# Kernel optimization log

Measured on AMD Instinct MI355X. Metric: run time of the kernel, lower is better.

Reference implementation:

```python
import jax, jax.numpy as jnp
import numpy as np

B, S, H = 16, 512, 768
NH, DH = 12, 64  # heads, head dim (H = NH*DH)
E = 8            # number of experts


def setup_inputs() -> dict:
    key = jax.random.key(0)
    ks = jax.random.split(key, 9)
    w_scale = 1.0 / np.sqrt(H).astype(np.float32)
    return {
        "hidden_states": jax.random.normal(ks[0], (B, S, H), jnp.float32),
        "attention_mask": jnp.zeros((B, 1, 1, S), jnp.float32),
        "Wq": jax.random.normal(ks[1], (E, H, H), jnp.float32) * w_scale,
        "bq": jnp.zeros((E, H), jnp.float32),
        "Wk": jax.random.normal(ks[2], (E, H, H), jnp.float32) * w_scale,
        "bk": jnp.zeros((E, H), jnp.float32),
        "Wv": jax.random.normal(ks[3], (E, H, H), jnp.float32) * w_scale,
        "bv": jnp.zeros((E, H), jnp.float32),
        "expert_idx": jax.random.randint(ks[4], (B,), 0, E, jnp.int64),
    }


def reference(hidden_states, attention_mask, Wq, bq, Wk, bk, Wv, bv, expert_idx):
    b, s, h = hidden_states.shape

    def proj(W, bias):
        # Per-sample expert selection: math-equivalent to computing all experts
        # then slice_for_expert, but gathers weights instead of activations.
        Wg = W[expert_idx]            # [B, H_out, H_in]
        bg = bias[expert_idx]         # [B, H_out]
        y = jnp.einsum('bsd,bod->bso', hidden_states, Wg) + bg[:, None, :]
        return y.reshape(b, s, NH, DH).transpose(0, 2, 1, 3)  # [B, NH, S, DH]

    q = proj(Wq, bq)
    k = proj(Wk, bk)
    v = proj(Wv, bv)

    scores = jnp.einsum('bhqd,bhkd->bhqk', q, k) / np.sqrt(DH).astype(np.float32)
    scores = scores + attention_mask
    probs = jax.nn.softmax(scores, axis=-1)  # dropout p=0.0 (eval)
    ctx = jnp.einsum('bhqk,bhkd->bhqd', probs, v)
    return ctx.transpose(0, 2, 1, 3).reshape(b, s, h)
```

## Files before the change

kernel.cpp:

```cpp
#include <hip/hip_runtime.h>
#include <hip/hip_bf16.h>
#include <stdint.h>

typedef __bf16 bf16;
typedef bf16 bf16x8 __attribute__((ext_vector_type(8)));
typedef bf16 bf16x4 __attribute__((ext_vector_type(4)));
typedef float f32x4 __attribute__((ext_vector_type(4)));

#define MFMA_16x16x32(a, b, c) __builtin_amdgcn_mfma_f32_16x16x32_bf16((a), (b), (c), 0, 0, 0)

constexpr int B = 16, S = 512, H = 768, NH = 12, DH = 64;
constexpr long NHID = (long)B * S * H;
constexpr long NW = (long)8 * H * H;

constexpr size_t XB_OFF = 0;
constexpr size_t XB_SZ  = (size_t)NHID * 2;
constexpr size_t W_SZ   = (size_t)NW * 2;
constexpr size_t WQ_OFF = XB_OFF + XB_SZ;
constexpr size_t WK_OFF = WQ_OFF + W_SZ;
constexpr size_t WV_OFF = WK_OFF + W_SZ;
constexpr size_t PROJ_SZ = (size_t)B * NH * S * DH * 2;
constexpr size_t QB_OFF = WV_OFF + W_SZ;
constexpr size_t KB_OFF = QB_OFF + PROJ_SZ;
constexpr size_t VB_OFF = KB_OFF + PROJ_SZ;
constexpr size_t WS_NEED = VB_OFF + PROJ_SZ;

__global__ void cvt_all(const float* __restrict__ x,
                        const float* __restrict__ wq, const float* __restrict__ wk,
                        const float* __restrict__ wv,
                        bf16* __restrict__ xb, bf16* __restrict__ wqb,
                        bf16* __restrict__ wkb, bf16* __restrict__ wvb) {
  long i = ((long)blockIdx.x * blockDim.x + threadIdx.x) * 8;
  const float* src;
  bf16* dst;
  long off;
  if (i < NHID)               { src = x;  dst = xb;  off = i; }
  else if (i < NHID + NW)     { src = wq; dst = wqb; off = i - NHID; }
  else if (i < NHID + 2 * NW) { src = wk; dst = wkb; off = i - NHID - NW; }
  else if (i < NHID + 3 * NW) { src = wv; dst = wvb; off = i - NHID - 2 * NW; }
  else return;
  const float4* sp = reinterpret_cast<const float4*>(src + off);
  float4 a = sp[0], b = sp[1];
  bf16x8 o;
  o[0] = (bf16)a.x; o[1] = (bf16)a.y; o[2] = (bf16)a.z; o[3] = (bf16)a.w;
  o[4] = (bf16)b.x; o[5] = (bf16)b.y; o[6] = (bf16)b.z; o[7] = (bf16)b.w;
  *reinterpret_cast<bf16x8*>(dst + off) = o;
}

__global__ __launch_bounds__(512, 2) void proj_gemm(
    const bf16* __restrict__ Xb,
    const bf16* __restrict__ Wqb, const bf16* __restrict__ Wkb, const bf16* __restrict__ Wvb,
    const float* __restrict__ bq, const float* __restrict__ bk, const float* __restrict__ bv,
    const int* __restrict__ eidx,
    bf16* __restrict__ Qb, bf16* __restrict__ Kb, bf16* __restrict__ Vb)
{
  __shared__ __align__(16) bf16 As[2][256 * 32];
  __shared__ __align__(16) bf16 Bs[2][128 * 32];

  const int xcd = blockIdx.x & 7;
  const int bi  = blockIdx.x >> 3;
  const int b   = xcd * 2 + (bi / 36);
  const int rem = bi % 36;
  const int m0  = (rem / 18) * 256;
  const int gy  = rem % 18;
  const int proj = gy / 6;
  const int n0 = (gy % 6) * 128;
  const int e = eidx[b];

  const bf16* W = (proj == 0 ? Wqb : (proj == 1 ? Wkb : Wvb)) + (size_t)e * H * H;
  const float* bias = (proj == 0 ? bq : (proj == 1 ? bk : bv)) + (size_t)e * H;
  bf16* Out = (proj == 0 ? Qb : (proj == 1 ? Kb : Vb));

  const int tid = threadIdx.x;
  const int lane = tid & 63;
  const int wave = tid >> 6;
  const int wm = wave >> 1, wn = wave & 1;
  const int r = lane & 15, lg = lane >> 4;

  const bf16* Abase = Xb + ((size_t)b * S + m0) * H;
  const bf16* Bbase = W + (size_t)n0 * H;

  const int srow = lane >> 2;
  const int sg = ((lane & 3) ^ ((lane >> 3) & 3)) * 8;

  auto stage = [&](int kt, int pb) {
    const int k0 = kt * 32;
#pragma unroll
    for (int i = 0; i < 2; ++i) {
      const int seg = wave * 2 + i;
      const bf16* ga = Abase + (size_t)(seg * 16 + srow) * H + k0 + sg;
      __builtin_amdgcn_global_load_lds(
          (const __attribute__((address_space(1))) void*)ga,
          (__attribute__((address_space(3))) void*)(&As[pb][seg * 512]), 16, 0, 0);
    }
    const bf16* gb = Bbase + (size_t)(wave * 16 + srow) * H + k0 + sg;
    __builtin_amdgcn_global_load_lds(
        (const __attribute__((address_space(1))) void*)gb,
        (__attribute__((address_space(3))) void*)(&Bs[pb][wave * 512]), 16, 0, 0);
  };

  f32x4 acc[4][4] = {};

  stage(0, 0);
  __syncthreads();

  const int sz = (r >> 1) & 3;

  int buf = 0;
#pragma unroll 1
  for (int kt = 0; kt < 24; ++kt) {
    if (kt < 23) stage(kt + 1, buf ^ 1);

    bf16x8 af[4], bfr[4];
#pragma unroll
    for (int mi = 0; mi < 4; ++mi)
      af[mi] = *reinterpret_cast<const bf16x8*>(
          &As[buf][(wm * 64 + mi * 16 + r) * 32 + ((lg ^ sz) * 8)]);
#pragma unroll
    for (int ni = 0; ni < 4; ++ni)
      bfr[ni] = *reinterpret_cast<const bf16x8*>(
          &Bs[buf][(wn * 64 + ni * 16 + r) * 32 + ((lg ^ sz) * 8)]);
#pragma unroll
    for (int mi = 0; mi < 4; ++mi)
#pragma unroll
      for (int ni = 0; ni < 4; ++ni)
        acc[mi][ni] = MFMA_16x16x32(af[mi], bfr[ni], acc[mi][ni]);

    __syncthreads();
    buf ^= 1;
  }

  if (proj != 2) {
#pragma unroll
    for (int ni = 0; ni < 4; ++ni) {
      const int col = n0 + wn * 64 + ni * 16 + r;
      const int nh = col >> 6, dh = col & 63;
      const float bb = bias[col];
      bf16* orow = Out + ((size_t)b * NH + nh) * S * DH + dh;
#pragma unroll
      for (int mi = 0; mi < 4; ++mi) {
#pragma unroll
        for (int rr = 0; rr < 4; ++rr) {
          const int srow2 = m0 + wm * 64 + mi * 16 + lg * 4 + rr;
          orow[(size_t)srow2 * DH] = (bf16)(acc[mi][ni][rr] + bb);
        }
      }
    }
  } else {
#pragma unroll
    for (int ni = 0; ni < 4; ++ni) {
      const int col = n0 + wn * 64 + ni * 16 + r;
      const int nh = col >> 6, dh = col & 63;
      const float bb = bias[col];
      bf16* orow = Out + ((size_t)b * NH + nh) * DH * S + (size_t)dh * S;
#pragma unroll
      for (int mi = 0; mi < 4; ++mi) {
        bf16x4 v;
#pragma unroll
        for (int rr = 0; rr < 4; ++rr) v[rr] = (bf16)(acc[mi][ni][rr] + bb);
        *reinterpret_cast<bf16x4*>(orow + m0 + wm * 64 + mi * 16 + lg * 4) = v;
      }
    }
  }
}

__global__ __launch_bounds__(256, 4) void attn_kernel(
    const bf16* __restrict__ Qb, const bf16* __restrict__ Kb, const bf16* __restrict__ VTb,
    const float* __restrict__ mask, float* __restrict__ out)
{
  __shared__ __align__(16) bf16 Ks[2][64 * 64];
  __shared__ __align__(16) bf16 Vs[2][64 * 64];
  __shared__ float maskS[512];

  const int x = blockIdx.x;
  const int xcd = x & 7;
  const int grp = x >> 3;
  const int qblk = grp & 7;
  const int bh = (grp >> 3) * 8 + xcd;
  const int b = bh / NH;
  const int h = bh % NH;
  const int tid = threadIdx.x;
  const int wave = tid >> 6;
  const int lane = tid & 63;
  const int r = lane & 15, lg = lane >> 4;
  const int q0 = qblk * 64 + wave * 16;

  const bf16* Q  = Qb  + (size_t)bh * S * DH;
  const bf16* K  = Kb  + (size_t)bh * S * DH;
  const bf16* VT = VTb + (size_t)bh * DH * S;

  for (int i = tid; i < S; i += 256) maskS[i] = mask[b * S + i];

  const int srowoff = lane >> 3;
  const int sg = (lane & 7) ^ srowoff;

  auto stage = [&](int kt, int buf) {
    const int kb = kt * 64;
#pragma unroll
    for (int i = 0; i < 2; ++i) {
      const int c = wave * 2 + i;
      const int row = c * 8 + srowoff;
      const bf16* gk = K + (size_t)(kb + row) * DH + sg * 8;
      __builtin_amdgcn_global_load_lds(
          (const __attribute__((address_space(1))) void*)gk,
          (__attribute__((address_space(3))) void*)(&Ks[buf][c * 512]), 16, 0, 0);
      const bf16* gv = VT + (size_t)row * S + kb + sg * 8;
      __builtin_amdgcn_global_load_lds(
          (const __attribute__((address_space(1))) void*)gv,
          (__attribute__((address_space(3))) void*)(&Vs[buf][c * 512]), 16, 0, 0);
    }
  };

  const bf16x8 qf0 = *reinterpret_cast<const bf16x8*>(&Q[(size_t)(q0 + r) * DH + lg * 8]);
  const bf16x8 qf1 = *reinterpret_cast<const bf16x8*>(&Q[(size_t)(q0 + r) * DH + 32 + lg * 8]);

  stage(0, 0);
  __syncthreads();

  float m = -3.0e38f, l = 0.0f;
  f32x4 ctx[4] = {};
  int buf = 0;

#pragma unroll 1
  for (int kt = 0; kt < 8; ++kt) {
    const int kb = kt * 64;
    if (kt < 7) stage(kt + 1, buf ^ 1);

    f32x4 sa[4];
#pragma unroll
    for (int t = 0; t < 4; ++t) {
      const int row = t * 16 + r;
      const int sw = row & 7;
      bf16x8 kf0 = *reinterpret_cast<const bf16x8*>(&Ks[buf][row * 64 + ((lg ^ sw) * 8)]);
      bf16x8 kf1 = *reinterpret_cast<const bf16x8*>(&Ks[buf][row * 64 + (((lg + 4) ^ sw) * 8)]);
      f32x4 a = {};
      a = MFMA_16x16x32(kf0, qf0, a);
      a = MFMA_16x16x32(kf1, qf1, a);
      sa[t] = a;
    }

    float tmax = -3.0e38f;
#pragma unroll
    for (int t = 0; t < 4; ++t)
#pragma unroll
      for (int rr = 0; rr < 4; ++rr) {
        float s = sa[t][rr] * 0.125f + maskS[kb + t * 16 + lg * 4 + rr];
        sa[t][rr] = s;
        tmax = fmaxf(tmax, s);
      }
    tmax = fmaxf(tmax, __shfl_xor(tmax, 16));
    tmax = fmaxf(tmax, __shfl_xor(tmax, 32));
    const float mnew = fmaxf(m, tmax);
    const float scale = __expf(m - mnew);
    m = mnew;
    float ps = 0.f;
#pragma unroll
    for (int t = 0; t < 4; ++t)
#pragma unroll
      for (int rr = 0; rr < 4; ++rr) {
        float p = __expf(sa[t][rr] - mnew);
        sa[t][rr] = p;
        ps += p;
      }
    l = l * scale + ps;
#pragma unroll
    for (int dt = 0; dt < 4; ++dt) ctx[dt] *= scale;

#pragma unroll
    for (int kc = 0; kc < 2; ++kc) {
      bf16x8 pf;
      f32x4 p0 = sa[2 * kc], p1 = sa[2 * kc + 1];
      pf[0] = (bf16)p0[0]; pf[1] = (bf16)p0[1]; pf[2] = (bf16)p0[2]; pf[3] = (bf16)p0[3];
      pf[4] = (bf16)p1[0]; pf[5] = (bf16)p1[1]; pf[6] = (bf16)p1[2]; pf[7] = (bf16)p1[3];
      const int chunk_lo = kc * 4 + (lg >> 1);
      const int rem = (lg & 1) * 4;
#pragma unroll
      for (int dt = 0; dt < 4; ++dt) {
        const int row = dt * 16 + r;
        const int sw = row & 7;
        const bf16* vlo = &Vs[buf][row * 64 + ((chunk_lo ^ sw) * 8) + rem];
        const bf16* vhi = &Vs[buf][row * 64 + (((chunk_lo + 2) ^ sw) * 8) + rem];
        bf16x4 lo = *reinterpret_cast<const bf16x4*>(vlo);
        bf16x4 hi = *reinterpret_cast<const bf16x4*>(vhi);
        bf16x8 vf;
        vf[0] = lo[0]; vf[1] = lo[1]; vf[2] = lo[2]; vf[3] = lo[3];
        vf[4] = hi[0]; vf[5] = hi[1]; vf[6] = hi[2]; vf[7] = hi[3];
        ctx[dt] = MFMA_16x16x32(vf, pf, ctx[dt]);
      }
    }

    __syncthreads();
    buf ^= 1;
  }

  l += __shfl_xor(l, 16);
  l += __shfl_xor(l, 32);
  const float inv = 1.0f / l;

  float* obase = out + ((size_t)b * S + q0 + r) * H + h * DH;
#pragma unroll
  for (int dt = 0; dt < 4; ++dt) {
    float4 o;
    o.x = ctx[dt][0] * inv; o.y = ctx[dt][1] * inv;
    o.z = ctx[dt][2] * inv; o.w = ctx[dt][3] * inv;
    *reinterpret_cast<float4*>(obase + dt * 16 + lg * 4) = o;
  }
}

extern "C" void kernel_launch(void* const* d_in, const int* in_sizes, int n_in,
                              void* d_out, int out_size, void* d_ws, size_t ws_size,
                              hipStream_t stream) {
  const float* hidden = (const float*)d_in[0];
  const float* mask   = (const float*)d_in[1];
  const float* Wq = (const float*)d_in[2];
  const float* bq = (const float*)d_in[3];
  const float* Wk = (const float*)d_in[4];
  const float* bk = (const float*)d_in[5];
  const float* Wv = (const float*)d_in[6];
  const float* bv = (const float*)d_in[7];
  const int* eidx = (const int*)d_in[8];

  if (ws_size < WS_NEED) return;

  char* ws = (char*)d_ws;
  bf16* Xb  = (bf16*)(ws + XB_OFF);
  bf16* Wqb = (bf16*)(ws + WQ_OFF);
  bf16* Wkb = (bf16*)(ws + WK_OFF);
  bf16* Wvb = (bf16*)(ws + WV_OFF);
  bf16* Qbf = (bf16*)(ws + QB_OFF);
  bf16* Kbf = (bf16*)(ws + KB_OFF);
  bf16* Vbf = (bf16*)(ws + VB_OFF);
  float* out = (float*)d_out;

  cvt_all<<<9984, 256, 0, stream>>>(hidden, Wq, Wk, Wv, Xb, Wqb, Wkb, Wvb);
  proj_gemm<<<576, 512, 0, stream>>>(Xb, Wqb, Wkb, Wvb, bq, bk, bv, eidx,
                                     Qbf, Kbf, Vbf);
  attn_kernel<<<1536, 256, 0, stream>>>(Qbf, Kbf, Vbf, mask, out);
}
```

Measured before the change: 102.9 us.

## Retile projection GEMM to 128x192 with triple-buffered 64-wide K pipeline

Changes the projection GEMM tile from 256x128 to 128x192, which raises the grid from 576 to 768 blocks, and doubles the K step to 64 over 12 iterations. LDS staging moves from double to triple buffering, with two stages in flight and hand-written s_waitcnt vmcnt/s_barrier in place of __syncthreads. MFMA bursts are wrapped in s_setprio. The aim is to hide global-to-LDS latency better and balance the work across CUs. In exchange it uses more LDS per block, and the exact vmcnt counts are fragile.

```diff
diff --git a/kernel.cpp b/kernel.cpp
--- a/kernel.cpp
+++ b/kernel.cpp
@@ -54,17 +54,18 @@
     const int* __restrict__ eidx,
     bf16* __restrict__ Qb, bf16* __restrict__ Kb, bf16* __restrict__ Vb)
 {
-  __shared__ __align__(16) bf16 As[2][256 * 32];
-  __shared__ __align__(16) bf16 Bs[2][128 * 32];
+  __shared__ __align__(16) bf16 As[3][2 * 128 * 32];
+  __shared__ __align__(16) bf16 Bs[3][2 * 192 * 32];
 
   const int xcd = blockIdx.x & 7;
   const int bi  = blockIdx.x >> 3;
-  const int b   = xcd * 2 + (bi / 36);
-  const int rem = bi % 36;
-  const int m0  = (rem / 18) * 256;
-  const int gy  = rem % 18;
-  const int proj = gy / 6;
-  const int n0 = (gy % 6) * 128;
+  const int b   = xcd * 2 + (bi / 48);
+  const int rem = bi % 48;
+  const int mt  = rem / 12;
+  const int nt  = rem % 12;
+  const int m0  = mt * 128;
+  const int proj = nt >> 2;
+  const int n0  = (nt & 3) * 192;
   const int e = eidx[b];
 
   const bf16* W = (proj == 0 ? Wqb : (proj == 1 ? Wkb : Wvb)) + (size_t)e * H * H;
@@ -74,7 +75,7 @@
   const int tid = threadIdx.x;
   const int lane = tid & 63;
   const int wave = tid >> 6;
-  const int wm = wave >> 1, wn = wave & 1;
+  const int wm = wave >> 2, wn = wave & 3;
   const int r = lane & 15, lg = lane >> 4;
 
   const bf16* Abase = Xb + ((size_t)b * S + m0) * H;
@@ -84,56 +85,77 @@
   const int sg = ((lane & 3) ^ ((lane >> 3) & 3)) * 8;
 
   auto stage = [&](int kt, int pb) {
-    const int k0 = kt * 32;
+    const int k0 = kt * 64;
 #pragma unroll
     for (int i = 0; i < 2; ++i) {
-      const int seg = wave * 2 + i;
-      const bf16* ga = Abase + (size_t)(seg * 16 + srow) * H + k0 + sg;
+      const int u = wave * 2 + i;
+      const int kh = u >> 3, p = u & 7;
+      const bf16* ga = Abase + (size_t)(p * 16 + srow) * H + k0 + kh * 32 + sg;
       __builtin_amdgcn_global_load_lds(
           (const __attribute__((address_space(1))) void*)ga,
-          (__attribute__((address_space(3))) void*)(&As[pb][seg * 512]), 16, 0, 0);
-    }
-    const bf16* gb = Bbase + (size_t)(wave * 16 + srow) * H + k0 + sg;
-    __builtin_amdgcn_global_load_lds(
-        (const __attribute__((address_space(1))) void*)gb,
-        (__attribute__((address_space(3))) void*)(&Bs[pb][wave * 512]), 16, 0, 0);
+          (__attribute__((address_space(3))) void*)(&As[pb][u * 512]), 16, 0, 0);
+    }
+#pragma unroll
+    for (int i = 0; i < 3; ++i) {
+      const int u = wave * 3 + i;
+      const int kh = u / 12, p = u % 12;
+      const bf16* gb = Bbase + (size_t)(p * 16 + srow) * H + k0 + kh * 32 + sg;
+      __builtin_amdgcn_global_load_lds(
+          (const __attribute__((address_space(1))) void*)gb,
+          (__attribute__((address_space(3))) void*)(&Bs[pb][u * 512]), 16, 0, 0);
+    }
   };
 
-  f32x4 acc[4][4] = {};
+  f32x4 acc[4][3] = {};
 
   stage(0, 0);
-  __syncthreads();
+  stage(1, 1);
+  asm volatile("s_waitcnt vmcnt(5) lgkmcnt(0)\n\ts_barrier" ::: "memory");
 
   const int sz = (r >> 1) & 3;
 
-  int buf = 0;
+  int buf = 0, nb = 2;
 #pragma unroll 1
-  for (int kt = 0; kt < 24; ++kt) {
-    if (kt < 23) stage(kt + 1, buf ^ 1);
-
-    bf16x8 af[4], bfr[4];
-#pragma unroll
-    for (int mi = 0; mi < 4; ++mi)
-      af[mi] = *reinterpret_cast<const bf16x8*>(
-          &As[buf][(wm * 64 + mi * 16 + r) * 32 + ((lg ^ sz) * 8)]);
-#pragma unroll
-    for (int ni = 0; ni < 4; ++ni)
-      bfr[ni] = *reinterpret_cast<const bf16x8*>(
-          &Bs[buf][(wn * 64 + ni * 16 + r) * 32 + ((lg ^ sz) * 8)]);
-#pragma unroll
-    for (int mi = 0; mi < 4; ++mi)
-#pragma unroll
-      for (int ni = 0; ni < 4; ++ni)
-        acc[mi][ni] = MFMA_16x16x32(af[mi], bfr[ni], acc[mi][ni]);
-
-    __syncthreads();
-    buf ^= 1;
+  for (int t = 0; t < 12; ++t) {
+    if (t + 2 < 12) stage(t + 2, nb);
+
+    const bf16* Ab = &As[buf][0];
+    const bf16* Bb = &Bs[buf][0];
+#pragma unroll
+    for (int kh = 0; kh < 2; ++kh) {
+      bf16x8 bfr[3];
+#pragma unroll
+      for (int ni = 0; ni < 3; ++ni)
+        bfr[ni] = *reinterpret_cast<const bf16x8*>(
+            &Bb[kh * 6144 + (wn * 48 + ni * 16 + r) * 32 + ((lg ^ sz) * 8)]);
+#pragma unroll
+      for (int half = 0; half < 2; ++half) {
+        bf16x8 af0 = *reinterpret_cast<const bf16x8*>(
+            &Ab[kh * 4096 + (wm * 64 + (half * 2) * 16 + r) * 32 + ((lg ^ sz) * 8)]);
+        bf16x8 af1 = *reinterpret_cast<const bf16x8*>(
+            &Ab[kh * 4096 + (wm * 64 + (half * 2 + 1) * 16 + r) * 32 + ((lg ^ sz) * 8)]);
+        __builtin_amdgcn_s_setprio(1);
+#pragma unroll
+        for (int ni = 0; ni < 3; ++ni) {
+          acc[half * 2][ni]     = MFMA_16x16x32(af0, bfr[ni], acc[half * 2][ni]);
+          acc[half * 2 + 1][ni] = MFMA_16x16x32(af1, bfr[ni], acc[half * 2 + 1][ni]);
+        }
+        __builtin_amdgcn_s_setprio(0);
+      }
+    }
+
+    if (t < 10)
+      asm volatile("s_waitcnt vmcnt(5) lgkmcnt(0)\n\ts_barrier" ::: "memory");
+    else if (t == 10)
+      asm volatile("s_waitcnt vmcnt(0) lgkmcnt(0)\n\ts_barrier" ::: "memory");
+    buf = (buf == 2) ? 0 : buf + 1;
+    nb  = (nb == 2) ? 0 : nb + 1;
   }
 
   if (proj != 2) {
 #pragma unroll
-    for (int ni = 0; ni < 4; ++ni) {
-      const int col = n0 + wn * 64 + ni * 16 + r;
+    for (int ni = 0; ni < 3; ++ni) {
+      const int col = n0 + wn * 48 + ni * 16 + r;
       const int nh = col >> 6, dh = col & 63;
       const float bb = bias[col];
       bf16* orow = Out + ((size_t)b * NH + nh) * S * DH + dh;
@@ -148,8 +170,8 @@
     }
   } else {
 #pragma unroll
-    for (int ni = 0; ni < 4; ++ni) {
-      const int col = n0 + wn * 64 + ni * 16 + r;
+    for (int ni = 0; ni < 3; ++ni) {
+      const int col = n0 + wn * 48 + ni * 16 + r;
       const int nh = col >> 6, dh = col & 63;
       const float bb = bias[col];
       bf16* orow = Out + ((size_t)b * NH + nh) * DH * S + (size_t)dh * S;
@@ -333,7 +355,7 @@
   float* out = (float*)d_out;
 
   cvt_all<<<9984, 256, 0, stream>>>(hidden, Wq, Wk, Wv, Xb, Wqb, Wkb, Wvb);
-  proj_gemm<<<576, 512, 0, stream>>>(Xb, Wqb, Wkb, Wvb, bq, bk, bv, eidx,
+  proj_gemm<<<768, 512, 0, stream>>>(Xb, Wqb, Wkb, Wvb, bq, bk, bv, eidx,
                                      Qbf, Kbf, Vbf);
   attn_kernel<<<1536, 256, 0, stream>>>(Qbf, Kbf, Vbf, mask, out);
 }
```

Result: slower. 109.8 us (+6.7%).

## Fuse fp32-to-bf16 conversion into projection GEMM tile loads

Applied to the files above, without the earlier changes.

Drops the separate conversion kernel that wrote bf16 copies of the hidden states and all expert weights, and instead loads fp32 tiles straight into registers inside the projection GEMM. There they are packed to bf16 and written into swizzled LDS buffers. This avoids converting all 8 experts' weights when only the selected ones are used, and removes a launch plus a full write and re-read of the intermediates. In exchange the GEMM reads twice as many bytes per tile, uses register prefetch two steps ahead instead of async global-to-LDS loads, and raises wave priority around the MFMA block.

```diff
diff --git a/kernel.cpp b/kernel.cpp
--- a/kernel.cpp
+++ b/kernel.cpp
@@ -10,46 +10,16 @@
 #define MFMA_16x16x32(a, b, c) __builtin_amdgcn_mfma_f32_16x16x32_bf16((a), (b), (c), 0, 0, 0)
 
 constexpr int B = 16, S = 512, H = 768, NH = 12, DH = 64;
-constexpr long NHID = (long)B * S * H;
-constexpr long NW = (long)8 * H * H;
-
-constexpr size_t XB_OFF = 0;
-constexpr size_t XB_SZ  = (size_t)NHID * 2;
-constexpr size_t W_SZ   = (size_t)NW * 2;
-constexpr size_t WQ_OFF = XB_OFF + XB_SZ;
-constexpr size_t WK_OFF = WQ_OFF + W_SZ;
-constexpr size_t WV_OFF = WK_OFF + W_SZ;
+
 constexpr size_t PROJ_SZ = (size_t)B * NH * S * DH * 2;
-constexpr size_t QB_OFF = WV_OFF + W_SZ;
+constexpr size_t QB_OFF = 0;
 constexpr size_t KB_OFF = QB_OFF + PROJ_SZ;
 constexpr size_t VB_OFF = KB_OFF + PROJ_SZ;
 constexpr size_t WS_NEED = VB_OFF + PROJ_SZ;
 
-__global__ void cvt_all(const float* __restrict__ x,
-                        const float* __restrict__ wq, const float* __restrict__ wk,
-                        const float* __restrict__ wv,
-                        bf16* __restrict__ xb, bf16* __restrict__ wqb,
-                        bf16* __restrict__ wkb, bf16* __restrict__ wvb) {
-  long i = ((long)blockIdx.x * blockDim.x + threadIdx.x) * 8;
-  const float* src;
-  bf16* dst;
-  long off;
-  if (i < NHID)               { src = x;  dst = xb;  off = i; }
-  else if (i < NHID + NW)     { src = wq; dst = wqb; off = i - NHID; }
-  else if (i < NHID + 2 * NW) { src = wk; dst = wkb; off = i - NHID - NW; }
-  else if (i < NHID + 3 * NW) { src = wv; dst = wvb; off = i - NHID - 2 * NW; }
-  else return;
-  const float4* sp = reinterpret_cast<const float4*>(src + off);
-  float4 a = sp[0], b = sp[1];
-  bf16x8 o;
-  o[0] = (bf16)a.x; o[1] = (bf16)a.y; o[2] = (bf16)a.z; o[3] = (bf16)a.w;
-  o[4] = (bf16)b.x; o[5] = (bf16)b.y; o[6] = (bf16)b.z; o[7] = (bf16)b.w;
-  *reinterpret_cast<bf16x8*>(dst + off) = o;
-}
-
 __global__ __launch_bounds__(512, 2) void proj_gemm(
-    const bf16* __restrict__ Xb,
-    const bf16* __restrict__ Wqb, const bf16* __restrict__ Wkb, const bf16* __restrict__ Wvb,
+    const float* __restrict__ Xf,
+    const float* __restrict__ Wqf, const float* __restrict__ Wkf, const float* __restrict__ Wvf,
     const float* __restrict__ bq, const float* __restrict__ bk, const float* __restrict__ bv,
     const int* __restrict__ eidx,
     bf16* __restrict__ Qb, bf16* __restrict__ Kb, bf16* __restrict__ Vb)
@@ -67,7 +37,7 @@
   const int n0 = (gy % 6) * 128;
   const int e = eidx[b];
 
-  const bf16* W = (proj == 0 ? Wqb : (proj == 1 ? Wkb : Wvb)) + (size_t)e * H * H;
+  const float* W = (proj == 0 ? Wqf : (proj == 1 ? Wkf : Wvf)) + (size_t)e * H * H;
   const float* bias = (proj == 0 ? bq : (proj == 1 ? bk : bv)) + (size_t)e * H;
   bf16* Out = (proj == 0 ? Qb : (proj == 1 ? Kb : Vb));
 
@@ -77,40 +47,50 @@
   const int wm = wave >> 1, wn = wave & 1;
   const int r = lane & 15, lg = lane >> 4;
 
-  const bf16* Abase = Xb + ((size_t)b * S + m0) * H;
-  const bf16* Bbase = W + (size_t)n0 * H;
-
-  const int srow = lane >> 2;
-  const int sg = ((lane & 3) ^ ((lane >> 3) & 3)) * 8;
-
-  auto stage = [&](int kt, int pb) {
-    const int k0 = kt * 32;
-#pragma unroll
-    for (int i = 0; i < 2; ++i) {
-      const int seg = wave * 2 + i;
-      const bf16* ga = Abase + (size_t)(seg * 16 + srow) * H + k0 + sg;
-      __builtin_amdgcn_global_load_lds(
-          (const __attribute__((address_space(1))) void*)ga,
-          (__attribute__((address_space(3))) void*)(&As[pb][seg * 512]), 16, 0, 0);
-    }
-    const bf16* gb = Bbase + (size_t)(wave * 16 + srow) * H + k0 + sg;
-    __builtin_amdgcn_global_load_lds(
-        (const __attribute__((address_space(1))) void*)gb,
-        (__attribute__((address_space(3))) void*)(&Bs[pb][wave * 512]), 16, 0, 0);
+  const int rowA = tid >> 1, ha = tid & 1;
+  const int rowB = tid >> 2, qB = tid & 3;
+  const float* gA = Xf + ((size_t)b * S + m0 + rowA) * H + ha * 16;
+  const float* gB = W + (size_t)(n0 + rowB) * H + qB * 8;
+  const int sA = (rowA >> 1) & 3, sB = (rowB >> 1) & 3;
+  const int slotA0 = ((ha * 2)     ^ sA) * 8;
+  const int slotA1 = ((ha * 2 + 1) ^ sA) * 8;
+  const int slotB  = (qB ^ sB) * 8;
+
+  f32x4 la0, la1, la2, la3, lb0, lb1;
+  auto loads = [&](int kt) {
+    const float* a = gA + kt * 32;
+    la0 = *reinterpret_cast<const f32x4*>(a);
+    la1 = *reinterpret_cast<const f32x4*>(a + 4);
+    la2 = *reinterpret_cast<const f32x4*>(a + 8);
+    la3 = *reinterpret_cast<const f32x4*>(a + 12);
+    const float* bb = gB + kt * 32;
+    lb0 = *reinterpret_cast<const f32x4*>(bb);
+    lb1 = *reinterpret_cast<const f32x4*>(bb + 4);
   };
+  auto pack = [](f32x4 x, f32x4 y) {
+    bf16x8 o;
+    o[0] = (bf16)x[0]; o[1] = (bf16)x[1]; o[2] = (bf16)x[2]; o[3] = (bf16)x[3];
+    o[4] = (bf16)y[0]; o[5] = (bf16)y[1]; o[6] = (bf16)y[2]; o[7] = (bf16)y[3];
+    return o;
+  };
+  auto writeT = [&](int pb) {
+    *reinterpret_cast<bf16x8*>(&As[pb][rowA * 32 + slotA0]) = pack(la0, la1);
+    *reinterpret_cast<bf16x8*>(&As[pb][rowA * 32 + slotA1]) = pack(la2, la3);
+    *reinterpret_cast<bf16x8*>(&Bs[pb][rowB * 32 + slotB])  = pack(lb0, lb1);
+  };
 
   f32x4 acc[4][4] = {};
 
-  stage(0, 0);
-  __syncthreads();
+  loads(0);
+  writeT(0);
+  loads(1);
+  asm volatile("s_waitcnt lgkmcnt(0)\n\ts_barrier" ::: "memory");
 
   const int sz = (r >> 1) & 3;
 
   int buf = 0;
 #pragma unroll 1
   for (int kt = 0; kt < 24; ++kt) {
-    if (kt < 23) stage(kt + 1, buf ^ 1);
-
     bf16x8 af[4], bfr[4];
 #pragma unroll
     for (int mi = 0; mi < 4; ++mi)
@@ -120,13 +100,19 @@
     for (int ni = 0; ni < 4; ++ni)
       bfr[ni] = *reinterpret_cast<const bf16x8*>(
           &Bs[buf][(wn * 64 + ni * 16 + r) * 32 + ((lg ^ sz) * 8)]);
+    __builtin_amdgcn_s_setprio(1);
 #pragma unroll
     for (int mi = 0; mi < 4; ++mi)
 #pragma unroll
       for (int ni = 0; ni < 4; ++ni)
         acc[mi][ni] = MFMA_16x16x32(af[mi], bfr[ni], acc[mi][ni]);
-
-    __syncthreads();
+    __builtin_amdgcn_s_setprio(0);
+
+    if (kt < 23) {
+      writeT(buf ^ 1);
+      if (kt < 22) loads(kt + 2);
+      asm volatile("s_waitcnt lgkmcnt(0)\n\ts_barrier" ::: "memory");
+    }
     buf ^= 1;
   }
 
@@ -323,17 +309,12 @@
   if (ws_size < WS_NEED) return;
 
   char* ws = (char*)d_ws;
-  bf16* Xb  = (bf16*)(ws + XB_OFF);
-  bf16* Wqb = (bf16*)(ws + WQ_OFF);
-  bf16* Wkb = (bf16*)(ws + WK_OFF);
-  bf16* Wvb = (bf16*)(ws + WV_OFF);
   bf16* Qbf = (bf16*)(ws + QB_OFF);
   bf16* Kbf = (bf16*)(ws + KB_OFF);
   bf16* Vbf = (bf16*)(ws + VB_OFF);
   float* out = (float*)d_out;
 
-  cvt_all<<<9984, 256, 0, stream>>>(hidden, Wq, Wk, Wv, Xb, Wqb, Wkb, Wvb);
-  proj_gemm<<<576, 512, 0, stream>>>(Xb, Wqb, Wkb, Wvb, bq, bk, bv, eidx,
+  proj_gemm<<<576, 512, 0, stream>>>(hidden, Wq, Wk, Wv, bq, bk, bv, eidx,
                                      Qbf, Kbf, Vbf);
   attn_kernel<<<1536, 256, 0, stream>>>(Qbf, Kbf, Vbf, mask, out);
 }
```

Result: faster. 100.4 us (-2.4%).

## Fuse weight fp32-to-bf16 conversion into projection GEMM operand loads

Applied to the files above, without the earlier changes.

The separate conversion pass over all expert weights is dropped. The projection GEMM now streams fp32 weights straight into LDS and converts them to bf16 in registers before the MFMAs. The point is to avoid converting weights for all 8 experts when only the selected ones are used, and to save a full read and write of the weight tensors. In exchange, the GEMM reads twice as many weight bytes, needs a larger LDS buffer (which may hurt occupancy), and does extra convert instructions. It also raises wave priority around the MFMA block.

```diff
diff --git a/kernel.cpp b/kernel.cpp
--- a/kernel.cpp
+++ b/kernel.cpp
@@ -11,51 +11,35 @@
 
 constexpr int B = 16, S = 512, H = 768, NH = 12, DH = 64;
 constexpr long NHID = (long)B * S * H;
-constexpr long NW = (long)8 * H * H;
 
 constexpr size_t XB_OFF = 0;
 constexpr size_t XB_SZ  = (size_t)NHID * 2;
-constexpr size_t W_SZ   = (size_t)NW * 2;
-constexpr size_t WQ_OFF = XB_OFF + XB_SZ;
-constexpr size_t WK_OFF = WQ_OFF + W_SZ;
-constexpr size_t WV_OFF = WK_OFF + W_SZ;
 constexpr size_t PROJ_SZ = (size_t)B * NH * S * DH * 2;
-constexpr size_t QB_OFF = WV_OFF + W_SZ;
+constexpr size_t QB_OFF = XB_OFF + XB_SZ;
 constexpr size_t KB_OFF = QB_OFF + PROJ_SZ;
 constexpr size_t VB_OFF = KB_OFF + PROJ_SZ;
 constexpr size_t WS_NEED = VB_OFF + PROJ_SZ;
 
-__global__ void cvt_all(const float* __restrict__ x,
-                        const float* __restrict__ wq, const float* __restrict__ wk,
-                        const float* __restrict__ wv,
-                        bf16* __restrict__ xb, bf16* __restrict__ wqb,
-                        bf16* __restrict__ wkb, bf16* __restrict__ wvb) {
+__global__ void cvt_x(const float* __restrict__ src, bf16* __restrict__ dst) {
   long i = ((long)blockIdx.x * blockDim.x + threadIdx.x) * 8;
-  const float* src;
-  bf16* dst;
-  long off;
-  if (i < NHID)               { src = x;  dst = xb;  off = i; }
-  else if (i < NHID + NW)     { src = wq; dst = wqb; off = i - NHID; }
-  else if (i < NHID + 2 * NW) { src = wk; dst = wkb; off = i - NHID - NW; }
-  else if (i < NHID + 3 * NW) { src = wv; dst = wvb; off = i - NHID - 2 * NW; }
-  else return;
-  const float4* sp = reinterpret_cast<const float4*>(src + off);
+  if (i >= NHID) return;
+  const float4* sp = reinterpret_cast<const float4*>(src + i);
   float4 a = sp[0], b = sp[1];
   bf16x8 o;
   o[0] = (bf16)a.x; o[1] = (bf16)a.y; o[2] = (bf16)a.z; o[3] = (bf16)a.w;
   o[4] = (bf16)b.x; o[5] = (bf16)b.y; o[6] = (bf16)b.z; o[7] = (bf16)b.w;
-  *reinterpret_cast<bf16x8*>(dst + off) = o;
+  *reinterpret_cast<bf16x8*>(dst + i) = o;
 }
 
 __global__ __launch_bounds__(512, 2) void proj_gemm(
     const bf16* __restrict__ Xb,
-    const bf16* __restrict__ Wqb, const bf16* __restrict__ Wkb, const bf16* __restrict__ Wvb,
+    const float* __restrict__ Wqf, const float* __restrict__ Wkf, const float* __restrict__ Wvf,
     const float* __restrict__ bq, const float* __restrict__ bk, const float* __restrict__ bv,
     const int* __restrict__ eidx,
     bf16* __restrict__ Qb, bf16* __restrict__ Kb, bf16* __restrict__ Vb)
 {
-  __shared__ __align__(16) bf16 As[2][256 * 32];
-  __shared__ __align__(16) bf16 Bs[2][128 * 32];
+  __shared__ __align__(16) bf16  As[2][256 * 32];
+  __shared__ __align__(16) float Bsf[2][128 * 32];
 
   const int xcd = blockIdx.x & 7;
   const int bi  = blockIdx.x >> 3;
@@ -67,7 +51,7 @@
   const int n0 = (gy % 6) * 128;
   const int e = eidx[b];
 
-  const bf16* W = (proj == 0 ? Wqb : (proj == 1 ? Wkb : Wvb)) + (size_t)e * H * H;
+  const float* W = (proj == 0 ? Wqf : (proj == 1 ? Wkf : Wvf)) + (size_t)e * H * H;
   const float* bias = (proj == 0 ? bq : (proj == 1 ? bk : bv)) + (size_t)e * H;
   bf16* Out = (proj == 0 ? Qb : (proj == 1 ? Kb : Vb));
 
@@ -78,25 +62,31 @@
   const int r = lane & 15, lg = lane >> 4;
 
   const bf16* Abase = Xb + ((size_t)b * S + m0) * H;
-  const bf16* Bbase = W + (size_t)n0 * H;
-
-  const int srow = lane >> 2;
-  const int sg = ((lane & 3) ^ ((lane >> 3) & 3)) * 8;
+  const float* Bbase = W + (size_t)n0 * H;
+
+  const int srowA = lane >> 2;
+  const int sgA = ((lane & 3) ^ ((lane >> 3) & 3)) * 8;
+  const int srowB = lane >> 3;
+  const int sgB = ((lane & 7) ^ srowB) * 4;
 
   auto stage = [&](int kt, int pb) {
     const int k0 = kt * 32;
 #pragma unroll
     for (int i = 0; i < 2; ++i) {
       const int seg = wave * 2 + i;
-      const bf16* ga = Abase + (size_t)(seg * 16 + srow) * H + k0 + sg;
+      const bf16* ga = Abase + (size_t)(seg * 16 + srowA) * H + k0 + sgA;
       __builtin_amdgcn_global_load_lds(
           (const __attribute__((address_space(1))) void*)ga,
           (__attribute__((address_space(3))) void*)(&As[pb][seg * 512]), 16, 0, 0);
     }
-    const bf16* gb = Bbase + (size_t)(wave * 16 + srow) * H + k0 + sg;
-    __builtin_amdgcn_global_load_lds(
-        (const __attribute__((address_space(1))) void*)gb,
-        (__attribute__((address_space(3))) void*)(&Bs[pb][wave * 512]), 16, 0, 0);
+#pragma unroll
+    for (int i = 0; i < 2; ++i) {
+      const int u = wave * 2 + i;
+      const float* gb = Bbase + (size_t)(u * 8 + srowB) * H + k0 + sgB;
+      __builtin_amdgcn_global_load_lds(
+          (const __attribute__((address_space(1))) void*)gb,
+          (__attribute__((address_space(3))) void*)(&Bsf[pb][u * 256]), 16, 0, 0);
+    }
   };
 
   f32x4 acc[4][4] = {};
@@ -117,14 +107,23 @@
       af[mi] = *reinterpret_cast<const bf16x8*>(
           &As[buf][(wm * 64 + mi * 16 + r) * 32 + ((lg ^ sz) * 8)]);
 #pragma unroll
-    for (int ni = 0; ni < 4; ++ni)
-      bfr[ni] = *reinterpret_cast<const bf16x8*>(
-          &Bs[buf][(wn * 64 + ni * 16 + r) * 32 + ((lg ^ sz) * 8)]);
+    for (int ni = 0; ni < 4; ++ni) {
+      const int row = wn * 64 + ni * 16 + r;
+      const int k7 = row & 7;
+      f32x4 x0 = *reinterpret_cast<const f32x4*>(&Bsf[buf][row * 32 + (((lg * 2) ^ k7) * 4)]);
+      f32x4 x1 = *reinterpret_cast<const f32x4*>(&Bsf[buf][row * 32 + (((lg * 2 + 1) ^ k7) * 4)]);
+      bf16x8 o;
+      o[0] = (bf16)x0[0]; o[1] = (bf16)x0[1]; o[2] = (bf16)x0[2]; o[3] = (bf16)x0[3];
+      o[4] = (bf16)x1[0]; o[5] = (bf16)x1[1]; o[6] = (bf16)x1[2]; o[7] = (bf16)x1[3];
+      bfr[ni] = o;
+    }
+    __builtin_amdgcn_s_setprio(1);
 #pragma unroll
     for (int mi = 0; mi < 4; ++mi)
 #pragma unroll
       for (int ni = 0; ni < 4; ++ni)
         acc[mi][ni] = MFMA_16x16x32(af[mi], bfr[ni], acc[mi][ni]);
+    __builtin_amdgcn_s_setprio(0);
 
     __syncthreads();
     buf ^= 1;
@@ -324,16 +323,13 @@
 
   char* ws = (char*)d_ws;
   bf16* Xb  = (bf16*)(ws + XB_OFF);
-  bf16* Wqb = (bf16*)(ws + WQ_OFF);
-  bf16* Wkb = (bf16*)(ws + WK_OFF);
-  bf16* Wvb = (bf16*)(ws + WV_OFF);
   bf16* Qbf = (bf16*)(ws + QB_OFF);
   bf16* Kbf = (bf16*)(ws + KB_OFF);
   bf16* Vbf = (bf16*)(ws + VB_OFF);
   float* out = (float*)d_out;
 
-  cvt_all<<<9984, 256, 0, stream>>>(hidden, Wq, Wk, Wv, Xb, Wqb, Wkb, Wvb);
-  proj_gemm<<<576, 512, 0, stream>>>(Xb, Wqb, Wkb, Wvb, bq, bk, bv, eidx,
+  cvt_x<<<3072, 256, 0, stream>>>(hidden, Xb);
+  proj_gemm<<<576, 512, 0, stream>>>(Xb, Wq, Wk, Wv, bq, bk, bv, eidx,
                                      Qbf, Kbf, Vbf);
   attn_kernel<<<1536, 256, 0, stream>>>(Qbf, Kbf, Vbf, mask, out);
 }
```

New measurement: 126.4 us. 22.8% more time.
